# Kernel tuning notes

Measured on AMD Instinct MI355X. Metric: run time of the kernel, lower is better.

Reference implementation:

```python
import jax, jax.numpy as jnp
import numpy as np

B, T, D = 2, 2048, 1024
H = 16
HD = D // H  # 64


def _rope_tables(t_len, hd, dtype=jnp.float32):
    inv_freq = 1.0 / (10000.0 ** (jnp.arange(0, hd, 2, dtype=jnp.float32) / hd))
    freqs = jnp.outer(jnp.arange(t_len, dtype=jnp.float32), inv_freq)  # [T, hd/2]
    emb = jnp.concatenate([freqs, freqs], axis=-1)  # [T, hd]
    return emb.astype(dtype)


def _rotate_half(x):
    x1, x2 = jnp.split(x, 2, axis=-1)
    return jnp.concatenate([-x2, x1], axis=-1)


def setup_inputs() -> dict:
    key = jax.random.key(0)
    k1, k2, k3 = jax.random.split(key, 3)
    x = jax.random.normal(k1, (B, T, D), dtype=jnp.float32)
    w_qkv = jax.random.normal(k2, (D, 3 * D), dtype=jnp.float32) * (D ** -0.5)
    w_out = jax.random.normal(k3, (D, D), dtype=jnp.float32) * (D ** -0.5)
    return {"x": x, "w_qkv": w_qkv, "w_out": w_out}


def reference(x, w_qkv, w_out):
    Bc, Tc, Dc = x.shape
    scale = HD ** -0.5
    qkv = x @ w_qkv  # [B,T,3D]
    q, k, v = jnp.split(qkv, 3, axis=-1)
    # -> [B,H,T,hd]
    q = q.reshape(Bc, Tc, H, HD).transpose(0, 2, 1, 3)
    k = k.reshape(Bc, Tc, H, HD).transpose(0, 2, 1, 3)
    v = v.reshape(Bc, Tc, H, HD).transpose(0, 2, 1, 3)
    emb = _rope_tables(Tc, HD, x.dtype)  # [T,hd]
    cos = jnp.cos(emb)[None, None, :, :]
    sin = jnp.sin(emb)[None, None, :, :]
    q = q * cos + _rotate_half(q) * sin
    k = k * cos + _rotate_half(k) * sin
    attn = jnp.einsum('bhqd,bhkd->bhqk', q, k) * scale  # [B,H,T,T]
    causal = jnp.tril(jnp.ones((Tc, Tc), dtype=bool))
    attn = jnp.where(causal[None, None], attn, -jnp.inf)
    attn = jax.nn.softmax(attn, axis=-1)
    out = jnp.einsum('bhqk,bhkd->bhqd', attn, v)
    out = out.transpose(0, 2, 1, 3).reshape(Bc, Tc, Dc)
    return out @ w_out
```

## Files before the change

### kernel.cpp

```cpp
#include <hip/hip_runtime.h>

#define TSEQ 2048
#define DMODEL 1024
#define NHEAD 16
#define HDIM 64
#define NB 2
#define MROWS 4096
#define NQKV 3072
#define QSCALE 0.1803368801111204f
#define ROPE_C (13.2877123795494f / 32.0f)
#define NEGINF -3.0e38f

using s16x8 = __attribute__((ext_vector_type(8))) short;
using s16x4 = __attribute__((ext_vector_type(4))) short;
using f32x4 = __attribute__((ext_vector_type(4))) float;
using u32x2 = __attribute__((ext_vector_type(2))) unsigned int;

static __device__ __forceinline__ float b2f(unsigned short u) {
  union { unsigned int i; float f; } x; x.i = ((unsigned int)u) << 16; return x.f;
}
static __device__ __forceinline__ unsigned short f2b(float f) {
  unsigned int u = __float_as_uint(f);
  u += 0x7fffu + ((u >> 16) & 1u);
  return (unsigned short)(u >> 16);
}

typedef const __attribute__((address_space(1))) char gchar;
typedef __attribute__((address_space(3))) char lchar;
static __device__ __forceinline__ void gload_lds16(const void* g, void* l) {
  __builtin_amdgcn_global_load_lds((gchar*)g, (lchar*)l, 16, 0, 0);
}

__global__ __launch_bounds__(256) void k_prep(const float* __restrict__ x,
                                              short* __restrict__ xb,
                                              const float* __restrict__ wq,
                                              short* __restrict__ wqT,
                                              const float* __restrict__ wo,
                                              short* __restrict__ woT) {
  __shared__ float tile[32][33];
  const int blk = blockIdx.x;
  const int tid = threadIdx.x;
  if (blk < 4096) {
    const int i = blk * 256 + tid;
    const float4 v = ((const float4*)x)[i];
    s16x4 o;
    o.x = (short)f2b(v.x); o.y = (short)f2b(v.y);
    o.z = (short)f2b(v.z); o.w = (short)f2b(v.w);
    ((s16x4*)xb)[i] = o;
    return;
  }
  const float* in; short* out; int C, bx, by;
  if (blk < 7168) {
    const int l = blk - 4096; in = wq; out = wqT; C = NQKV;
    bx = l % 96; by = l / 96;
  } else {
    const int l = blk - 7168; in = wo; out = woT; C = DMODEL;
    bx = l & 31; by = l >> 5;
  }
  const int tx = tid & 31, ty4 = (tid >> 5) * 4;
#pragma unroll
  for (int i = 0; i < 4; ++i)
    tile[ty4 + i][tx] = in[(by * 32 + ty4 + i) * C + bx * 32 + tx];
  __syncthreads();
#pragma unroll
  for (int i = 0; i < 4; ++i)
    out[(bx * 32 + ty4 + i) * DMODEL + by * 32 + tx] = (short)f2b(tile[tx][ty4 + i]);
}

__global__ __launch_bounds__(256) void k_gemm_qkv(const short* __restrict__ A,
                                                  const short* __restrict__ BT,
                                                  short* __restrict__ Qo,
                                                  short* __restrict__ Ko,
                                                  short* __restrict__ Vt) {
  __shared__ __attribute__((aligned(16))) short As[128 * 64];
  __shared__ __attribute__((aligned(16))) short Bs[128 * 64];
  const int K = DMODEL;
  const int tid = threadIdx.x;
  const int wave = tid >> 6, lane = tid & 63, quad = lane >> 4, l15 = lane & 15;
  const int wm = (wave >> 1) * 64, wn = (wave & 1) * 64;
  const int m0 = blockIdx.y * 128, n0 = blockIdx.x * 128;
  f32x4 acc[4][4] = {};
  const char* Ab = (const char*)A;
  const char* Bb = (const char*)BT;
  char* AsB = (char*)As;
  char* BsB = (char*)Bs;
  int srow[4], sg[4];
#pragma unroll
  for (int p = 0; p < 4; ++p) {
    const int i = p * 256 + tid;
    srow[p] = i >> 3;
    sg[p] = (i & 7) ^ (srow[p] & 7);
  }
  for (int k0 = 0; k0 < K; k0 += 64) {
    __syncthreads();
#pragma unroll
    for (int p = 0; p < 4; ++p) {
      const long go = ((long)(m0 + srow[p]) * K + k0) * 2 + sg[p] * 16;
      gload_lds16(Ab + go, AsB + p * 4096 + wave * 1024);
    }
#pragma unroll
    for (int p = 0; p < 4; ++p) {
      const long go = ((long)(n0 + srow[p]) * K + k0) * 2 + sg[p] * 16;
      gload_lds16(Bb + go, BsB + p * 4096 + wave * 1024);
    }
    __syncthreads();
#pragma unroll
    for (int hf = 0; hf < 2; ++hf) {
      s16x8 af[4], bf[4];
#pragma unroll
      for (int i = 0; i < 4; ++i) {
        const int ra = wm + i * 16 + l15;
        af[i] = *(const s16x8*)(AsB + ra * 128 + (((hf * 4 + quad) ^ (ra & 7)) * 16));
        const int rb = wn + i * 16 + l15;
        bf[i] = *(const s16x8*)(BsB + rb * 128 + (((hf * 4 + quad) ^ (rb & 7)) * 16));
      }
#pragma unroll
      for (int i = 0; i < 4; ++i)
#pragma unroll
        for (int j = 0; j < 4; ++j)
          acc[i][j] = __builtin_amdgcn_mfma_f32_16x16x32_bf16(af[i], bf[j], acc[i][j], 0, 0, 0);
    }
  }
  const int colbase = n0 + wn;
  const int region = colbase >> 10;
  const int hh = (colbase & 1023) >> 6;
  const int bq = m0 >> 11;
  const int tbase = (m0 & 2047) + wm;
  if (region == 2) {
    short* dst = Vt + (((long)(bq * NHEAD + hh) * HDIM) << 11);
#pragma unroll
    for (int i = 0; i < 4; ++i) {
      const int t0 = tbase + i * 16 + quad * 4;
#pragma unroll
      for (int j = 0; j < 4; ++j) {
        const int d = j * 16 + l15;
        s16x4 w;
        w.x = (short)f2b(acc[i][j][0]);
        w.y = (short)f2b(acc[i][j][1]);
        w.z = (short)f2b(acc[i][j][2]);
        w.w = (short)f2b(acc[i][j][3]);
        *(s16x4*)(dst + (((long)d) << 11) + t0) = w;
      }
    }
  } else {
    short* dst = (region ? Ko : Qo) + (long)(bq * NHEAD + hh) * TSEQ * HDIM;
#pragma unroll
    for (int i = 0; i < 4; ++i)
#pragma unroll
      for (int j = 0; j < 4; ++j) {
        const int d = j * 16 + l15;
#pragma unroll
        for (int r = 0; r < 4; ++r) {
          const int t = tbase + i * 16 + quad * 4 + r;
          dst[(long)t * HDIM + d] = (short)f2b(acc[i][j][r]);
        }
      }
  }
}

__global__ __launch_bounds__(256) void k_ropek(short* __restrict__ Kp) {
  const int tt = blockIdx.x, bh = blockIdx.y;
  const int tid = threadIdx.x;
  const int row = tid >> 2, chunk = tid & 3;
  const int t = tt * 64 + row;
  short* base = Kp + ((long)bh * TSEQ + t) * HDIM + chunk * 8;
  const s16x8 lo = *(const s16x8*)base;
  const s16x8 hi = *(const s16x8*)(base + 32);
  s16x8 nlo, nhi;
  const float tf = (float)t;
#pragma unroll
  for (int j = 0; j < 8; ++j) {
    const float inv = exp2f(-(float)(chunk * 8 + j) * ROPE_C);
    float sn, cs;
    __sincosf(tf * inv, &sn, &cs);
    const float a = b2f((unsigned short)lo[j]);
    const float b = b2f((unsigned short)hi[j]);
    nlo[j] = (short)f2b(a * cs - b * sn);
    nhi[j] = (short)f2b(b * cs + a * sn);
  }
  *(s16x8*)base = nlo;
  *(s16x8*)(base + 32) = nhi;
}

template <int IM, bool OUT_BF16>
__global__ __launch_bounds__(256) void k_gemm(const short* __restrict__ A,
                                              const short* __restrict__ BT,
                                              void* __restrict__ Cv,
                                              int M, int N, int K) {
  __shared__ __attribute__((aligned(16))) short As[IM * 32 * 64];
  __shared__ __attribute__((aligned(16))) short Bs[128 * 64];
  const int tid = threadIdx.x;
  const int wave = tid >> 6, lane = tid & 63, quad = lane >> 4, l15 = lane & 15;
  const int wm = (wave >> 1) * (IM * 16), wn = (wave & 1) * 64;
  const int m0 = blockIdx.y * (IM * 32), n0 = blockIdx.x * 128;
  f32x4 acc[IM][4] = {};
  const char* Ab = (const char*)A;
  const char* Bb = (const char*)BT;
  char* AsB = (char*)As;
  char* BsB = (char*)Bs;
  int srow[4], sg[4];
#pragma unroll
  for (int p = 0; p < 4; ++p) {
    const int i = p * 256 + tid;
    srow[p] = i >> 3;
    sg[p] = (i & 7) ^ (srow[p] & 7);
  }
  for (int k0 = 0; k0 < K; k0 += 64) {
    __syncthreads();
#pragma unroll
    for (int p = 0; p < IM; ++p) {
      const long go = ((long)(m0 + srow[p]) * K + k0) * 2 + sg[p] * 16;
      gload_lds16(Ab + go, AsB + p * 4096 + wave * 1024);
    }
#pragma unroll
    for (int p = 0; p < 4; ++p) {
      const long go = ((long)(n0 + srow[p]) * K + k0) * 2 + sg[p] * 16;
      gload_lds16(Bb + go, BsB + p * 4096 + wave * 1024);
    }
    __syncthreads();
#pragma unroll
    for (int hf = 0; hf < 2; ++hf) {
      s16x8 af[IM], bf[4];
#pragma unroll
      for (int i = 0; i < IM; ++i) {
        const int ra = wm + i * 16 + l15;
        af[i] = *(const s16x8*)(AsB + ra * 128 + (((hf * 4 + quad) ^ (ra & 7)) * 16));
      }
#pragma unroll
      for (int j = 0; j < 4; ++j) {
        const int rb = wn + j * 16 + l15;
        bf[j] = *(const s16x8*)(BsB + rb * 128 + (((hf * 4 + quad) ^ (rb & 7)) * 16));
      }
#pragma unroll
      for (int i = 0; i < IM; ++i)
#pragma unroll
        for (int j = 0; j < 4; ++j)
          acc[i][j] = __builtin_amdgcn_mfma_f32_16x16x32_bf16(af[i], bf[j], acc[i][j], 0, 0, 0);
    }
  }
#pragma unroll
  for (int i = 0; i < IM; ++i) {
    const int row = m0 + wm + i * 16 + quad * 4;
#pragma unroll
    for (int j = 0; j < 4; ++j) {
      const int col = n0 + wn + j * 16 + l15;
#pragma unroll
      for (int r = 0; r < 4; ++r) {
        if (OUT_BF16) ((short*)Cv)[(long)(row + r) * N + col] = (short)f2b(acc[i][j][r]);
        else          ((float*)Cv)[(long)(row + r) * N + col] = acc[i][j][r];
      }
    }
  }
}

__global__ __launch_bounds__(512) __attribute__((amdgpu_waves_per_eu(4)))
void k_attn(const short* __restrict__ Qg,
            const short* __restrict__ Kg,
            const short* __restrict__ Vg,
            short* __restrict__ O) {
  __shared__ __attribute__((aligned(16))) short Ks[2][64 * 64];
  __shared__ __attribute__((aligned(16))) short Vs[2][64 * 64];
  __shared__ __attribute__((aligned(16))) short pl[8][16 * 64];
  const int bx = blockIdx.x, by = blockIdx.y;
  const int qi = ((by >> 4) & 1) ? (15 - bx) : bx;
  const int bh = by;
  const int b = bh >> 4, h = bh & 15;
  const int tid = threadIdx.x, wave = tid >> 6, lane = tid & 63;
  const int quad = lane >> 4, l15 = lane & 15;
  const char* Kb = (const char*)(Kg + (long)bh * TSEQ * HDIM);
  const char* Vb = (const char*)(Vg + (long)bh * HDIM * TSEQ);
  const short* Qb = Qg + (long)bh * TSEQ * HDIM;
  const int qr0 = qi * 128 + wave * 16;
  const s16x8 rq0 = *(const s16x8*)&Qb[(qr0 + l15) * HDIM + quad * 8];
  const s16x8 rq1 = *(const s16x8*)&Qb[(qr0 + l15) * HDIM + 32 + quad * 8];
  s16x8 aq0, aq1;
  {
    const float tf = (float)(qr0 + l15);
#pragma unroll
    for (int j = 0; j < 8; ++j) {
      const float inv = exp2f(-(float)(quad * 8 + j) * ROPE_C);
      float sn, cs;
      __sincosf(tf * inv, &sn, &cs);
      sn *= QSCALE; cs *= QSCALE;
      const float q0 = b2f((unsigned short)rq0[j]);
      const float q1 = b2f((unsigned short)rq1[j]);
      aq0[j] = (short)f2b(q0 * cs - q1 * sn);
      aq1[j] = (short)f2b(q1 * cs + q0 * sn);
    }
  }
  f32x4 o[4] = {};
  float lsum = 0.0f;
  const int kr0 = tid >> 3, kg0 = (tid & 7) ^ (kr0 & 7);
  char* KsB = (char*)Ks;
  char* VsB = (char*)Vs;
  char* plwB = (char*)pl + wave * 2048;
  const int ldsw = wave * 1024;

#define STAGE(kjv, buf)                                                     \
  do {                                                                      \
    gload_lds16(Kb + (kjv) * 8192 + (kr0 * 8 + kg0) * 16,                   \
                KsB + (buf) * 8192 + ldsw);                                 \
    gload_lds16(Vb + (kjv) * 128 + kr0 * (TSEQ * 2) + kg0 * 16,             \
                VsB + (buf) * 8192 + ldsw);                                 \
  } while (0)

  STAGE(0, 0);
  __syncthreads();

  const int kjmax = 2 * qi + 1;
  const int kjd = qr0 >> 6;
  for (int kj = 0; kj <= kjmax; ++kj) {
    const int cur = kj & 1;
    if (kj < kjmax) STAGE(kj + 1, cur ^ 1);
    if (kj <= kjd) {
      const char* kb = KsB + cur * 8192;
      const char* vb = VsB + cur * 8192;
      f32x4 s[4];
#pragma unroll
      for (int j2 = 0; j2 < 4; ++j2) {
        const int row = j2 * 16 + l15;
        const s16x8 k0 = *(const s16x8*)(kb + row * 128 + ((quad ^ (row & 7)) * 16));
        const s16x8 k1 = *(const s16x8*)(kb + row * 128 + (((4 + quad) ^ (row & 7)) * 16));
        f32x4 z = {};
        z = __builtin_amdgcn_mfma_f32_16x16x32_bf16(k0, aq0, z, 0, 0, 0);
        z = __builtin_amdgcn_mfma_f32_16x16x32_bf16(k1, aq1, z, 0, 0, 0);
        s[j2] = z;
      }
      if (kj == kjd) {
        const int qloc = (qr0 & 63) + l15;
#pragma unroll
        for (int j2 = 0; j2 < 4; ++j2)
#pragma unroll
          for (int r = 0; r < 4; ++r)
            if (j2 * 16 + quad * 4 + r > qloc) s[j2][r] = NEGINF;
      }
      float ps = 0.0f;
#pragma unroll
      for (int j2 = 0; j2 < 4; ++j2) {
        const unsigned int u0 = __float_as_uint(exp2f(s[j2][0])) & 0xffff0000u;
        const unsigned int u1 = __float_as_uint(exp2f(s[j2][1])) & 0xffff0000u;
        const unsigned int u2 = __float_as_uint(exp2f(s[j2][2])) & 0xffff0000u;
        const unsigned int u3 = __float_as_uint(exp2f(s[j2][3])) & 0xffff0000u;
        ps += __uint_as_float(u0) + __uint_as_float(u1) +
              __uint_as_float(u2) + __uint_as_float(u3);
        u32x2 w;
        w.x = (u0 >> 16) | u1;
        w.y = (u2 >> 16) | u3;
        const int t0 = j2 * 16 + quad * 4;
        *(u32x2*)(plwB + l15 * 128 + (((t0 >> 3) ^ (l15 & 7)) * 16) + (quad & 1) * 8) = w;
      }
      lsum += ps;
      const s16x8 bp0 = *(const s16x8*)(plwB + l15 * 128 + ((quad ^ (l15 & 7)) * 16));
      const s16x8 bp1 = *(const s16x8*)(plwB + l15 * 128 + (((4 + quad) ^ (l15 & 7)) * 16));
#pragma unroll
      for (int hs = 0; hs < 4; ++hs) {
        const int d = hs * 16 + l15;
        const s16x8 av0 = *(const s16x8*)(vb + d * 128 + ((quad ^ (d & 7)) * 16));
        const s16x8 av1 = *(const s16x8*)(vb + d * 128 + (((4 + quad) ^ (d & 7)) * 16));
        o[hs] = __builtin_amdgcn_mfma_f32_16x16x32_bf16(av0, bp0, o[hs], 0, 0, 0);
        o[hs] = __builtin_amdgcn_mfma_f32_16x16x32_bf16(av1, bp1, o[hs], 0, 0, 0);
      }
    }
    __syncthreads();
  }
#undef STAGE
  lsum += __shfl_xor(lsum, 16);
  lsum += __shfl_xor(lsum, 32);
  const float rinv = 1.0f / lsum;
  const int t = qr0 + l15;
  short* Orow = O + (long)(b * TSEQ + t) * DMODEL + h * HDIM + quad * 4;
#pragma unroll
  for (int hs = 0; hs < 4; ++hs) {
    s16x4 w;
    w.x = (short)f2b(o[hs][0] * rinv);
    w.y = (short)f2b(o[hs][1] * rinv);
    w.z = (short)f2b(o[hs][2] * rinv);
    w.w = (short)f2b(o[hs][3] * rinv);
    *(s16x4*)(Orow + hs * 16) = w;
  }
}

extern "C" void kernel_launch(void* const* d_in, const int* in_sizes, int n_in,
                              void* d_out, int out_size, void* d_ws, size_t ws_size,
                              hipStream_t stream) {
  const float* x = (const float*)d_in[0];
  const float* w_qkv = (const float*)d_in[1];
  const float* w_out = (const float*)d_in[2];
  float* out = (float*)d_out;
  char* ws = (char*)d_ws;

  short* xb    = (short*)(ws);
  short* wqkvT = (short*)(ws + (8ll << 20));
  short* woutT = (short*)(ws + (14ll << 20));
  short* Qb    = (short*)(ws + (16ll << 20));
  short* Kb    = (short*)(ws + (24ll << 20));
  short* Vt    = (short*)(ws + (32ll << 20));
  short* Ob    = (short*)(ws + (40ll << 20));

  k_prep<<<dim3(8192), dim3(256), 0, stream>>>(x, xb, w_qkv, wqkvT, w_out, woutT);
  k_gemm_qkv<<<dim3(NQKV / 128, MROWS / 128), dim3(256), 0, stream>>>(
      xb, wqkvT, Qb, Kb, Vt);
  k_ropek<<<dim3(TSEQ / 64, NB * NHEAD), dim3(256), 0, stream>>>(Kb);
  k_attn<<<dim3(TSEQ / 128, NB * NHEAD), dim3(512), 0, stream>>>(Qb, Kb, Vt, Ob);
  k_gemm<2, false><<<dim3(DMODEL / 128, MROWS / 64), dim3(256), 0, stream>>>(
      Ob, woutT, (void*)out, MROWS, DMODEL, DMODEL);
}
```

Measured before the change: 193.9 us.

## Fuse K RoPE into QKV GEMM epilogue and restructure attention per-wave heads

Applies RoPE to K inside the QKV GEMM epilogue in fp32 and removes the separate k_ropek kernel and its extra read/write pass. The attention kernel is rewritten so each wave owns a different head and processes two 16-row query tiles. K and V fragments are loaded straight from global memory into registers instead of through double-buffered shared memory with barriers. Row sums are computed with an MFMA against a ones vector, and a hardware exp2 builtin is used when available. This trades shared-memory reuse and coalesced staging for fewer barriers and fewer launches, at the risk of redundant and less efficient global loads.

```diff
diff --git a/kernel.cpp b/kernel.cpp
--- a/kernel.cpp
+++ b/kernel.cpp
@@ -24,6 +24,12 @@
   u += 0x7fffu + ((u >> 16) & 1u);
   return (unsigned short)(u >> 16);
 }
+
+#if __has_builtin(__builtin_amdgcn_exp2f)
+#define EXP2(x) __builtin_amdgcn_exp2f(x)
+#else
+#define EXP2(x) exp2f(x)
+#endif
 
 typedef const __attribute__((address_space(1))) char gchar;
 typedef __attribute__((address_space(3))) char lchar;
@@ -143,6 +149,25 @@
       }
     }
   } else {
+    if (region == 1) {
+#pragma unroll
+      for (int i = 0; i < 4; ++i)
+#pragma unroll
+        for (int j = 0; j < 2; ++j) {
+          const int d = j * 16 + l15;
+          const float inv = exp2f(-(float)d * ROPE_C);
+#pragma unroll
+          for (int r = 0; r < 4; ++r) {
+            const int t = tbase + i * 16 + quad * 4 + r;
+            float sn, cs;
+            __sincosf((float)t * inv, &sn, &cs);
+            const float a = acc[i][j][r];
+            const float bv = acc[i][j + 2][r];
+            acc[i][j][r]     = a * cs - bv * sn;
+            acc[i][j + 2][r] = bv * cs + a * sn;
+          }
+        }
+    }
     short* dst = (region ? Ko : Qo) + (long)(bq * NHEAD + hh) * TSEQ * HDIM;
 #pragma unroll
     for (int i = 0; i < 4; ++i)
@@ -156,30 +181,6 @@
         }
       }
   }
-}
-
-__global__ __launch_bounds__(256) void k_ropek(short* __restrict__ Kp) {
-  const int tt = blockIdx.x, bh = blockIdx.y;
-  const int tid = threadIdx.x;
-  const int row = tid >> 2, chunk = tid & 3;
-  const int t = tt * 64 + row;
-  short* base = Kp + ((long)bh * TSEQ + t) * HDIM + chunk * 8;
-  const s16x8 lo = *(const s16x8*)base;
-  const s16x8 hi = *(const s16x8*)(base + 32);
-  s16x8 nlo, nhi;
-  const float tf = (float)t;
-#pragma unroll
-  for (int j = 0; j < 8; ++j) {
-    const float inv = exp2f(-(float)(chunk * 8 + j) * ROPE_C);
-    float sn, cs;
-    __sincosf(tf * inv, &sn, &cs);
-    const float a = b2f((unsigned short)lo[j]);
-    const float b = b2f((unsigned short)hi[j]);
-    nlo[j] = (short)f2b(a * cs - b * sn);
-    nhi[j] = (short)f2b(b * cs + a * sn);
-  }
-  *(s16x8*)base = nlo;
-  *(s16x8*)(base + 32) = nhi;
 }
 
 template <int IM, bool OUT_BF16>
@@ -253,130 +254,156 @@
   }
 }
 
-__global__ __launch_bounds__(512) __attribute__((amdgpu_waves_per_eu(4)))
-void k_attn(const short* __restrict__ Qg,
-            const short* __restrict__ Kg,
-            const short* __restrict__ Vg,
-            short* __restrict__ O) {
-  __shared__ __attribute__((aligned(16))) short Ks[2][64 * 64];
-  __shared__ __attribute__((aligned(16))) short Vs[2][64 * 64];
-  __shared__ __attribute__((aligned(16))) short pl[8][16 * 64];
-  const int bx = blockIdx.x, by = blockIdx.y;
-  const int qi = ((by >> 4) & 1) ? (15 - bx) : bx;
-  const int bh = by;
-  const int b = bh >> 4, h = bh & 15;
+
+static __device__ __forceinline__ void load_rope_q(const short* Qb, int row,
+                                                   int quad, s16x8* a0, s16x8* a1) {
+  const s16x8 r0 = *(const s16x8*)&Qb[row * HDIM + quad * 8];
+  const s16x8 r1 = *(const s16x8*)&Qb[row * HDIM + 32 + quad * 8];
+  const float tf = (float)row;
+  s16x8 o0, o1;
+#pragma unroll
+  for (int j = 0; j < 8; ++j) {
+    const float inv = exp2f(-(float)(quad * 8 + j) * ROPE_C);
+    float sn, cs;
+    __sincosf(tf * inv, &sn, &cs);
+    sn *= QSCALE; cs *= QSCALE;
+    const float q0 = b2f((unsigned short)r0[j]);
+    const float q1 = b2f((unsigned short)r1[j]);
+    o0[j] = (short)f2b(q0 * cs - q1 * sn);
+    o1[j] = (short)f2b(q1 * cs + q0 * sn);
+  }
+  *a0 = o0; *a1 = o1;
+}
+
+static __device__ __forceinline__ void pexp_store(char* plw, const f32x4* s,
+                                                  int quad, int l15) {
+#pragma unroll
+  for (int j2 = 0; j2 < 4; ++j2) {
+    const unsigned int u0 = __float_as_uint(EXP2(s[j2][0])) & 0xffff0000u;
+    const unsigned int u1 = __float_as_uint(EXP2(s[j2][1])) & 0xffff0000u;
+    const unsigned int u2 = __float_as_uint(EXP2(s[j2][2])) & 0xffff0000u;
+    const unsigned int u3 = __float_as_uint(EXP2(s[j2][3])) & 0xffff0000u;
+    u32x2 w;
+    w.x = (u0 >> 16) | u1;
+    w.y = (u2 >> 16) | u3;
+    const int t0 = j2 * 16 + quad * 4;
+    *(u32x2*)(plw + l15 * 128 + (((t0 >> 3) ^ (l15 & 7)) * 16) + (quad & 1) * 8) = w;
+  }
+}
+
+__global__ __launch_bounds__(256) void k_attn(const short* __restrict__ Qg,
+                                              const short* __restrict__ Kg,
+                                              const short* __restrict__ Vg,
+                                              short* __restrict__ O) {
+  __shared__ __attribute__((aligned(16))) short pl[4][2][16 * 64];
+  const int n = blockIdx.x;
+  const int gg = n & 7;
+  const int idx = n >> 3;
+  const int s = (idx < 32) ? (63 - idx) : (idx - 32);
   const int tid = threadIdx.x, wave = tid >> 6, lane = tid & 63;
   const int quad = lane >> 4, l15 = lane & 15;
+  const int bh = gg * 4 + wave;
+  const int b = bh >> 4, h = bh & 15;
+  const int qr0 = s * 32;
+  const int kd = (qr0 + 31) >> 6;
+  const short* Qb = Qg + (long)bh * TSEQ * HDIM;
   const char* Kb = (const char*)(Kg + (long)bh * TSEQ * HDIM);
   const char* Vb = (const char*)(Vg + (long)bh * HDIM * TSEQ);
-  const short* Qb = Qg + (long)bh * TSEQ * HDIM;
-  const int qr0 = qi * 128 + wave * 16;
-  const s16x8 rq0 = *(const s16x8*)&Qb[(qr0 + l15) * HDIM + quad * 8];
-  const s16x8 rq1 = *(const s16x8*)&Qb[(qr0 + l15) * HDIM + 32 + quad * 8];
-  s16x8 aq0, aq1;
+
+  s16x8 aqA0, aqA1, aqB0, aqB1;
+  load_rope_q(Qb, qr0 + l15, quad, &aqA0, &aqA1);
+  load_rope_q(Qb, qr0 + 16 + l15, quad, &aqB0, &aqB1);
+
+  s16x8 ones;
+#pragma unroll
+  for (int j = 0; j < 8; ++j) ones[j] = (short)0x3F80;
+
+  f32x4 oA[4] = {}, oB[4] = {}, zA = {}, zB = {};
+  char* plA = (char*)pl[wave][0];
+  char* plB = (char*)pl[wave][1];
+
+  for (int kj = 0; kj <= kd; ++kj) {
+    const char* kb = Kb + kj * 8192;
+    const char* vb = Vb + kj * 128;
+    s16x8 kf0[4], kf1[4], vf0[4], vf1[4];
+#pragma unroll
+    for (int j2 = 0; j2 < 4; ++j2) {
+      kf0[j2] = *(const s16x8*)(kb + (j2 * 16 + l15) * 128 + quad * 16);
+      kf1[j2] = *(const s16x8*)(kb + (j2 * 16 + l15) * 128 + 64 + quad * 16);
+    }
+#pragma unroll
+    for (int hs = 0; hs < 4; ++hs) {
+      vf0[hs] = *(const s16x8*)(vb + (hs * 16 + l15) * 4096 + quad * 16);
+      vf1[hs] = *(const s16x8*)(vb + (hs * 16 + l15) * 4096 + 64 + quad * 16);
+    }
+    f32x4 sA[4], sB[4];
+#pragma unroll
+    for (int j2 = 0; j2 < 4; ++j2) {
+      f32x4 z = {};
+      z = __builtin_amdgcn_mfma_f32_16x16x32_bf16(kf0[j2], aqA0, z, 0, 0, 0);
+      z = __builtin_amdgcn_mfma_f32_16x16x32_bf16(kf1[j2], aqA1, z, 0, 0, 0);
+      sA[j2] = z;
+      f32x4 y = {};
+      y = __builtin_amdgcn_mfma_f32_16x16x32_bf16(kf0[j2], aqB0, y, 0, 0, 0);
+      y = __builtin_amdgcn_mfma_f32_16x16x32_bf16(kf1[j2], aqB1, y, 0, 0, 0);
+      sB[j2] = y;
+    }
+    if (kj == kd) {
+      const int qA = (qr0 & 63) + l15;
+#pragma unroll
+      for (int j2 = 0; j2 < 4; ++j2)
+#pragma unroll
+        for (int r = 0; r < 4; ++r) {
+          const int tl = j2 * 16 + quad * 4 + r;
+          if (tl > qA) sA[j2][r] = NEGINF;
+          if (tl > qA + 16) sB[j2][r] = NEGINF;
+        }
+    }
+    pexp_store(plA, sA, quad, l15);
+    pexp_store(plB, sB, quad, l15);
+    const s16x8 bpA0 = *(const s16x8*)(plA + l15 * 128 + ((quad ^ (l15 & 7)) * 16));
+    const s16x8 bpA1 = *(const s16x8*)(plA + l15 * 128 + (((4 + quad) ^ (l15 & 7)) * 16));
+    const s16x8 bpB0 = *(const s16x8*)(plB + l15 * 128 + ((quad ^ (l15 & 7)) * 16));
+    const s16x8 bpB1 = *(const s16x8*)(plB + l15 * 128 + (((4 + quad) ^ (l15 & 7)) * 16));
+    zA = __builtin_amdgcn_mfma_f32_16x16x32_bf16(ones, bpA0, zA, 0, 0, 0);
+    zA = __builtin_amdgcn_mfma_f32_16x16x32_bf16(ones, bpA1, zA, 0, 0, 0);
+    zB = __builtin_amdgcn_mfma_f32_16x16x32_bf16(ones, bpB0, zB, 0, 0, 0);
+    zB = __builtin_amdgcn_mfma_f32_16x16x32_bf16(ones, bpB1, zB, 0, 0, 0);
+#pragma unroll
+    for (int hs = 0; hs < 4; ++hs) {
+      oA[hs] = __builtin_amdgcn_mfma_f32_16x16x32_bf16(vf0[hs], bpA0, oA[hs], 0, 0, 0);
+      oA[hs] = __builtin_amdgcn_mfma_f32_16x16x32_bf16(vf1[hs], bpA1, oA[hs], 0, 0, 0);
+      oB[hs] = __builtin_amdgcn_mfma_f32_16x16x32_bf16(vf0[hs], bpB0, oB[hs], 0, 0, 0);
+      oB[hs] = __builtin_amdgcn_mfma_f32_16x16x32_bf16(vf1[hs], bpB1, oB[hs], 0, 0, 0);
+    }
+  }
+  const float rA = 1.0f / zA[0];
+  const float rB = 1.0f / zB[0];
   {
-    const float tf = (float)(qr0 + l15);
-#pragma unroll
-    for (int j = 0; j < 8; ++j) {
-      const float inv = exp2f(-(float)(quad * 8 + j) * ROPE_C);
-      float sn, cs;
-      __sincosf(tf * inv, &sn, &cs);
-      sn *= QSCALE; cs *= QSCALE;
-      const float q0 = b2f((unsigned short)rq0[j]);
-      const float q1 = b2f((unsigned short)rq1[j]);
-      aq0[j] = (short)f2b(q0 * cs - q1 * sn);
-      aq1[j] = (short)f2b(q1 * cs + q0 * sn);
-    }
-  }
-  f32x4 o[4] = {};
-  float lsum = 0.0f;
-  const int kr0 = tid >> 3, kg0 = (tid & 7) ^ (kr0 & 7);
-  char* KsB = (char*)Ks;
-  char* VsB = (char*)Vs;
-  char* plwB = (char*)pl + wave * 2048;
-  const int ldsw = wave * 1024;
-
-#define STAGE(kjv, buf)                                                     \
-  do {                                                                      \
-    gload_lds16(Kb + (kjv) * 8192 + (kr0 * 8 + kg0) * 16,                   \
-                KsB + (buf) * 8192 + ldsw);                                 \
-    gload_lds16(Vb + (kjv) * 128 + kr0 * (TSEQ * 2) + kg0 * 16,             \
-                VsB + (buf) * 8192 + ldsw);                                 \
-  } while (0)
-
-  STAGE(0, 0);
-  __syncthreads();
-
-  const int kjmax = 2 * qi + 1;
-  const int kjd = qr0 >> 6;
-  for (int kj = 0; kj <= kjmax; ++kj) {
-    const int cur = kj & 1;
-    if (kj < kjmax) STAGE(kj + 1, cur ^ 1);
-    if (kj <= kjd) {
-      const char* kb = KsB + cur * 8192;
-      const char* vb = VsB + cur * 8192;
-      f32x4 s[4];
-#pragma unroll
-      for (int j2 = 0; j2 < 4; ++j2) {
-        const int row = j2 * 16 + l15;
-        const s16x8 k0 = *(const s16x8*)(kb + row * 128 + ((quad ^ (row & 7)) * 16));
-        const s16x8 k1 = *(const s16x8*)(kb + row * 128 + (((4 + quad) ^ (row & 7)) * 16));
-        f32x4 z = {};
-        z = __builtin_amdgcn_mfma_f32_16x16x32_bf16(k0, aq0, z, 0, 0, 0);
-        z = __builtin_amdgcn_mfma_f32_16x16x32_bf16(k1, aq1, z, 0, 0, 0);
-        s[j2] = z;
-      }
-      if (kj == kjd) {
-        const int qloc = (qr0 & 63) + l15;
-#pragma unroll
-        for (int j2 = 0; j2 < 4; ++j2)
-#pragma unroll
-          for (int r = 0; r < 4; ++r)
-            if (j2 * 16 + quad * 4 + r > qloc) s[j2][r] = NEGINF;
-      }
-      float ps = 0.0f;
-#pragma unroll
-      for (int j2 = 0; j2 < 4; ++j2) {
-        const unsigned int u0 = __float_as_uint(exp2f(s[j2][0])) & 0xffff0000u;
-        const unsigned int u1 = __float_as_uint(exp2f(s[j2][1])) & 0xffff0000u;
-        const unsigned int u2 = __float_as_uint(exp2f(s[j2][2])) & 0xffff0000u;
-        const unsigned int u3 = __float_as_uint(exp2f(s[j2][3])) & 0xffff0000u;
-        ps += __uint_as_float(u0) + __uint_as_float(u1) +
-              __uint_as_float(u2) + __uint_as_float(u3);
-        u32x2 w;
-        w.x = (u0 >> 16) | u1;
-        w.y = (u2 >> 16) | u3;
-        const int t0 = j2 * 16 + quad * 4;
-        *(u32x2*)(plwB + l15 * 128 + (((t0 >> 3) ^ (l15 & 7)) * 16) + (quad & 1) * 8) = w;
-      }
-      lsum += ps;
-      const s16x8 bp0 = *(const s16x8*)(plwB + l15 * 128 + ((quad ^ (l15 & 7)) * 16));
-      const s16x8 bp1 = *(const s16x8*)(plwB + l15 * 128 + (((4 + quad) ^ (l15 & 7)) * 16));
-#pragma unroll
-      for (int hs = 0; hs < 4; ++hs) {
-        const int d = hs * 16 + l15;
-        const s16x8 av0 = *(const s16x8*)(vb + d * 128 + ((quad ^ (d & 7)) * 16));
-        const s16x8 av1 = *(const s16x8*)(vb + d * 128 + (((4 + quad) ^ (d & 7)) * 16));
-        o[hs] = __builtin_amdgcn_mfma_f32_16x16x32_bf16(av0, bp0, o[hs], 0, 0, 0);
-        o[hs] = __builtin_amdgcn_mfma_f32_16x16x32_bf16(av1, bp1, o[hs], 0, 0, 0);
-      }
-    }
-    __syncthreads();
-  }
-#undef STAGE
-  lsum += __shfl_xor(lsum, 16);
-  lsum += __shfl_xor(lsum, 32);
-  const float rinv = 1.0f / lsum;
-  const int t = qr0 + l15;
-  short* Orow = O + (long)(b * TSEQ + t) * DMODEL + h * HDIM + quad * 4;
-#pragma unroll
-  for (int hs = 0; hs < 4; ++hs) {
-    s16x4 w;
-    w.x = (short)f2b(o[hs][0] * rinv);
-    w.y = (short)f2b(o[hs][1] * rinv);
-    w.z = (short)f2b(o[hs][2] * rinv);
-    w.w = (short)f2b(o[hs][3] * rinv);
-    *(s16x4*)(Orow + hs * 16) = w;
+    const int t = qr0 + l15;
+    short* Orow = O + (long)(b * TSEQ + t) * DMODEL + h * HDIM + quad * 4;
+#pragma unroll
+    for (int hs = 0; hs < 4; ++hs) {
+      s16x4 w;
+      w.x = (short)f2b(oA[hs][0] * rA);
+      w.y = (short)f2b(oA[hs][1] * rA);
+      w.z = (short)f2b(oA[hs][2] * rA);
+      w.w = (short)f2b(oA[hs][3] * rA);
+      *(s16x4*)(Orow + hs * 16) = w;
+    }
+  }
+  {
+    const int t = qr0 + 16 + l15;
+    short* Orow = O + (long)(b * TSEQ + t) * DMODEL + h * HDIM + quad * 4;
+#pragma unroll
+    for (int hs = 0; hs < 4; ++hs) {
+      s16x4 w;
+      w.x = (short)f2b(oB[hs][0] * rB);
+      w.y = (short)f2b(oB[hs][1] * rB);
+      w.z = (short)f2b(oB[hs][2] * rB);
+      w.w = (short)f2b(oB[hs][3] * rB);
+      *(s16x4*)(Orow + hs * 16) = w;
+    }
   }
 }
 
@@ -400,8 +427,7 @@
   k_prep<<<dim3(8192), dim3(256), 0, stream>>>(x, xb, w_qkv, wqkvT, w_out, woutT);
   k_gemm_qkv<<<dim3(NQKV / 128, MROWS / 128), dim3(256), 0, stream>>>(
       xb, wqkvT, Qb, Kb, Vt);
-  k_ropek<<<dim3(TSEQ / 64, NB * NHEAD), dim3(256), 0, stream>>>(Kb);
-  k_attn<<<dim3(TSEQ / 128, NB * NHEAD), dim3(512), 0, stream>>>(Qb, Kb, Vt, Ob);
+  k_attn<<<dim3(512), dim3(256), 0, stream>>>(Qb, Kb, Vt, Ob);
   k_gemm<2, false><<<dim3(DMODEL / 128, MROWS / 64), dim3(256), 0, stream>>>(
       Ob, woutT, (void*)out, MROWS, DMODEL, DMODEL);
 }
```

Measured after the change: 214.1 us. +10.4%, slower.
